# Kernel optimization log

Measured on AMD Instinct MI355X. Metric: run time of the kernel, lower is better.

Reference implementation:

```python
import jax, jax.numpy as jnp
import numpy as np

NUM_HEADS = 16


def setup_inputs() -> dict:
    key = jax.random.key(0)
    ks = jax.random.split(key, 9)
    B, N, C, R, T = 16, 1024, 1024, 64, 10
    s = 0.02
    x = jax.random.normal(ks[0], (B, N, C), dtype=jnp.float32)
    W_qkv = jax.random.normal(ks[1], (3 * C, C), dtype=jnp.float32) * s
    W_proj = jax.random.normal(ks[2], (C, C), dtype=jnp.float32) * s
    b_proj = jax.random.normal(ks[3], (C,), dtype=jnp.float32) * s
    A_k = jax.random.normal(ks[4], (T, R, C), dtype=jnp.float32) * s
    B_k = jax.random.normal(ks[5], (T, C, R), dtype=jnp.float32) * s
    A_v = jax.random.normal(ks[6], (T, R, C), dtype=jnp.float32) * s
    B_v = jax.random.normal(ks[7], (T, C, R), dtype=jnp.float32) * s
    return {"x": x, "W_qkv": W_qkv, "W_proj": W_proj, "b_proj": b_proj,
            "A_k": A_k, "B_k": B_k, "A_v": A_v, "B_v": B_v, "task": 4}


def reference(x, W_qkv, W_proj, b_proj, A_k, B_k, A_v, B_v, task):
    B, N, C = x.shape
    H = NUM_HEADS
    hd = C // H
    scale = hd ** (-0.5)

    # qkv projection: x @ W_qkv.T -> [B,N,3C] -> [3,B,H,N,hd]
    qkv = (x @ W_qkv.T).reshape(B, N, 3, H, hd).transpose(2, 0, 3, 1, 4)
    q, k, v = qkv[0], qkv[1], qkv[2]

    # merged LoRA weights: sum_{t<=task} B[t] @ A[t] -> [C, C]
    w_k = jnp.einsum('tcr,trd->cd', B_k[:task + 1], A_k[:task + 1])
    w_v = jnp.einsum('tcr,trd->cd', B_v[:task + 1], A_v[:task + 1])
    # F.linear(x, W) = x @ W.T ; reshape to [B,H,N,hd]
    dk = (x @ w_k.T).reshape(B, N, H, hd).transpose(0, 2, 1, 3)
    dv = (x @ w_v.T).reshape(B, N, H, hd).transpose(0, 2, 1, 3)
    k = k + dk
    v = v + dv

    attn = jax.nn.softmax(jnp.einsum('bhnd,bhmd->bhnm', q, k) * scale, axis=-1)
    out = jnp.einsum('bhnm,bhmd->bhnd', attn, v)
    out = out.transpose(0, 2, 1, 3).reshape(B, N, C)
    return out @ W_proj.T + b_proj
```

## Files before the change

### kernel.cpp

```cpp
#include <hip/hip_runtime.h>

typedef __attribute__((ext_vector_type(4))) float f32x4;
typedef __attribute__((ext_vector_type(8))) short s16x8;
typedef __attribute__((ext_vector_type(2))) unsigned int u32x2;
typedef __attribute__((ext_vector_type(4))) unsigned int u32x4;

#define LOG2E 1.44269504088896340736f

__device__ inline unsigned short f2b(float f) {
  unsigned int u = __float_as_uint(f);
  unsigned int r = (u + 0x7FFFu + ((u >> 16) & 1u)) >> 16;
  return (unsigned short)r;
}

__device__ inline unsigned int cvtpk_bf16(float lo, float hi) {
  unsigned int r;
  asm("v_cvt_pk_bf16_f32 %0, %1, %2" : "=v"(r) : "v"(lo), "v"(hi));
  return r;
}

__device__ inline void gload_lds16(const unsigned short* g, unsigned short* l) {
  __builtin_amdgcn_global_load_lds(
      (const __attribute__((address_space(1))) unsigned int*)g,
      (__attribute__((address_space(3))) unsigned int*)l, 16, 0, 0);
}

__global__ __launch_bounds__(256) void lora_merge(const float* __restrict__ A_k,
                                                  const float* __restrict__ B_k,
                                                  const float* __restrict__ A_v,
                                                  const float* __restrict__ B_v,
                                                  float* __restrict__ wk,
                                                  float* __restrict__ wv,
                                                  const int* __restrict__ taskp) {
  const float* A_ = blockIdx.y ? A_v : A_k;
  const float* B_ = blockIdx.y ? B_v : B_k;
  float* Wd = blockIdx.y ? wv : wk;
  __shared__ float Bs[64][65];
  __shared__ float As[64][65];
  const int tile = blockIdx.x;
  const int c0 = (tile >> 4) * 64, d0 = (tile & 15) * 64;
  const int tid = threadIdx.x;
  const int tx = tid & 15, ty = tid >> 4;
  const int T = *taskp + 1;
  float acc[4][4] = {};
  const int r = tid >> 2, cb = (tid & 3) * 16;
  for (int t = 0; t < T; ++t) {
    __syncthreads();
    const float* srcB = B_ + (size_t)t * 65536 + (size_t)(c0 + r) * 64 + cb;
    const float* srcA = A_ + (size_t)t * 65536 + (size_t)r * 1024 + d0 + cb;
#pragma unroll
    for (int j = 0; j < 16; j += 4) {
      f32x4 vb = *(const f32x4*)(srcB + j);
      Bs[r][cb + j] = vb.x; Bs[r][cb + j + 1] = vb.y;
      Bs[r][cb + j + 2] = vb.z; Bs[r][cb + j + 3] = vb.w;
      f32x4 va = *(const f32x4*)(srcA + j);
      As[r][cb + j] = va.x; As[r][cb + j + 1] = va.y;
      As[r][cb + j + 2] = va.z; As[r][cb + j + 3] = va.w;
    }
    __syncthreads();
#pragma unroll 8
    for (int rr = 0; rr < 64; ++rr) {
      float bv[4], av[4];
#pragma unroll
      for (int i = 0; i < 4; ++i) bv[i] = Bs[ty * 4 + i][rr];
#pragma unroll
      for (int j = 0; j < 4; ++j) av[j] = As[rr][tx * 4 + j];
#pragma unroll
      for (int i = 0; i < 4; ++i)
#pragma unroll
        for (int j = 0; j < 4; ++j) acc[i][j] += bv[i] * av[j];
    }
  }
#pragma unroll
  for (int i = 0; i < 4; ++i)
#pragma unroll
    for (int j = 0; j < 4; ++j)
      Wd[(size_t)(c0 + ty * 4 + i) * 1024 + d0 + tx * 4 + j] = acc[i][j];
}

__global__ void prep_all(const float* __restrict__ x, const float* __restrict__ Wproj,
                         const float* __restrict__ Wqkv, const float* __restrict__ wk,
                         const float* __restrict__ wv, unsigned short* __restrict__ xb,
                         unsigned short* __restrict__ Wp, unsigned short* __restrict__ Wc) {
  int i = blockIdx.x * 256 + threadIdx.x;
  f32x4 v;
  unsigned short* dst;
  int idx;
  if (i < 4194304) {
    idx = i; dst = xb;
    v = ((const f32x4*)x)[idx];
  } else if (i < 4456448) {
    idx = i - 4194304; dst = Wp;
    v = ((const f32x4*)Wproj)[idx];
  } else {
    idx = i - 4456448;
    dst = Wc;
    int e = idx * 4;
    v = *(const f32x4*)(Wqkv + e);
    int row = e >> 10;
    if (row >= 2048) {
      f32x4 d = *(const f32x4*)(wv + (e - 2097152));
      v = v + d;
    } else if (row >= 1024) {
      f32x4 d = *(const f32x4*)(wk + (e - 1048576));
      v = v + d;
    }
  }
  unsigned short o0 = f2b(v.x), o1 = f2b(v.y), o2 = f2b(v.z), o3 = f2b(v.w);
  unsigned long long pack = (unsigned long long)o0 | ((unsigned long long)o1 << 16) |
                            ((unsigned long long)o2 << 32) | ((unsigned long long)o3 << 48);
  ((unsigned long long*)dst)[idx] = pack;
}

template <int OUT_BF16, int ADD_BIAS, int VFUSE>
__global__ __launch_bounds__(512, 1) void gemm256(const unsigned short* __restrict__ A,
                                                  const unsigned short* __restrict__ B,
                                                  void* __restrict__ Cout,
                                                  const float* __restrict__ bias,
                                                  unsigned short* __restrict__ Vt,
                                                  int M, int N, int K) {
  __shared__ unsigned short SM[35840];
  const int tid = threadIdx.x;
  const int w = tid >> 6, l = tid & 63;
  const int lr = l & 15, lg = l >> 4;
  const int wm = w >> 2, wn = w & 3;

  const int lin = blockIdx.y * gridDim.x + blockIdx.x;
  const int cpx = (gridDim.x * gridDim.y) >> 3;
  const int s = (lin & 7) * cpx + (lin >> 3);
  const int bx = s % gridDim.x, by = s / gridDim.x;

  const int cs = tid ^ (((tid >> 5) & 1) << 1);
  const int r_st = ((cs >> 6) << 4) | ((cs >> 2) & 15);
  const int k_st = (cs & 3) << 3;
  const unsigned short* gA0 = A + (size_t)(by * 256 + r_st) * K + k_st;
  const unsigned short* gA1 = A + (size_t)(by * 256 + 128 + r_st) * K + k_st;
  const unsigned short* gB0 = B + (size_t)(bx * 256 + r_st) * K + k_st;
  const unsigned short* gB1 = B + (size_t)(bx * 256 + 128 + r_st) * K + k_st;
  const int wb = w * 512;

  const int swz = ((lr >> 3) & 1) << 4;
  const int fbase = lr * 32 + lg * 8;
  const int hA = wm * 4096;
  const int hB = (wn >> 1) * 4096;
  const int nb = (wn & 1) * 4;

  f32x4 acc[8][4] = {};
  const int NT = K >> 5;

#define SA_(t) (&SM[(t) * 8192])
#define SB_(t) (&SM[16384 + (t) * 8192])

  gload_lds16(gA0, SA_(0) + wb);
  gload_lds16(gA1, SA_(0) + 4096 + wb);
  gload_lds16(gB0, SB_(0) + wb);
  gload_lds16(gB1, SB_(0) + 4096 + wb);
  asm volatile("s_waitcnt vmcnt(0)" ::: "memory");
  __builtin_amdgcn_s_barrier();
  __builtin_amdgcn_sched_barrier(0);

  for (int t = 0; t < NT; ++t) {
    const int slot = t & 1;
    const int ts = (t + 1 < NT) ? (t + 1) : (NT - 1);
    const int ssl = (t + 1) & 1;
    const unsigned short* sa = SA_(slot) + hA;
    const unsigned short* sb = SB_(slot) + hB;
    gload_lds16(gA0 + ts * 32, SA_(ssl) + wb);
    gload_lds16(gA1 + ts * 32, SA_(ssl) + 4096 + wb);
    gload_lds16(gB0 + ts * 32, SB_(ssl) + wb);
    gload_lds16(gB1 + ts * 32, SB_(ssl) + 4096 + wb);
    s16x8 af[8], bf[2];
#pragma unroll
    for (int m = 0; m < 8; ++m)
      af[m] = *(const s16x8*)&sa[(m * 512 + fbase) ^ swz];
#pragma unroll
    for (int n = 0; n < 2; ++n)
      bf[n] = *(const s16x8*)&sb[((nb + n) * 512 + fbase) ^ swz];
    asm volatile("s_waitcnt lgkmcnt(0)" ::: "memory");
    __builtin_amdgcn_sched_barrier(0);
    __builtin_amdgcn_s_setprio(1);
#pragma unroll
    for (int m = 0; m < 8; ++m)
#pragma unroll
      for (int n = 0; n < 2; ++n)
        acc[m][n] = __builtin_amdgcn_mfma_f32_16x16x32_bf16(af[m], bf[n], acc[m][n], 0, 0, 0);
    __builtin_amdgcn_s_setprio(0);
    __builtin_amdgcn_sched_barrier(0);
#pragma unroll
    for (int n = 0; n < 2; ++n)
      bf[n] = *(const s16x8*)&sb[((nb + 2 + n) * 512 + fbase) ^ swz];
    asm volatile("s_waitcnt lgkmcnt(0)" ::: "memory");
    __builtin_amdgcn_sched_barrier(0);
    __builtin_amdgcn_s_setprio(1);
#pragma unroll
    for (int m = 0; m < 8; ++m)
#pragma unroll
      for (int n = 0; n < 2; ++n)
        acc[m][2 + n] = __builtin_amdgcn_mfma_f32_16x16x32_bf16(af[m], bf[n], acc[m][2 + n], 0, 0, 0);
    __builtin_amdgcn_s_setprio(0);
    __builtin_amdgcn_sched_barrier(0);
    asm volatile("s_waitcnt vmcnt(0)" ::: "memory");
    __builtin_amdgcn_s_barrier();
    __builtin_amdgcn_sched_barrier(0);
  }

  const int crow0 = by * 256 + wm * 128;
  const int ccol0 = bx * 256 + wn * 64;

  if (VFUSE) {
    unsigned short* Cq = (unsigned short*)Cout;
    if (bx < 8) {
      unsigned short* Cb = Cq + ((size_t)((ccol0 >> 10) & 1)) * 16777216;
#pragma unroll
      for (int m = 0; m < 8; ++m)
#pragma unroll
        for (int n = 0; n < 4; ++n)
#pragma unroll
          for (int rr = 0; rr < 4; ++rr) {
            int row = crow0 + m * 16 + lg * 4 + rr;
            int col = (ccol0 + n * 16 + lr) & 1023;
            Cb[(size_t)row * 1024 + col] = f2b(acc[m][n][rr]);
          }
    } else {
      asm volatile("s_waitcnt vmcnt(0)" ::: "memory");
      __syncthreads();
      unsigned int* T32 = (unsigned int*)SM;
      const int h0 = (bx - 8) * 4;
      const int bb = by >> 2;
      const int n_base = (by & 3) * 256;
#pragma unroll
      for (int hf = 0; hf < 2; ++hf) {
        if (wm == hf) {
#pragma unroll
          for (int m = 0; m < 8; ++m)
#pragma unroll
            for (int n = 0; n < 4; ++n) {
              int lcol = wn * 64 + n * 16 + lr;
              u32x2 pk;
              pk.x = (unsigned int)f2b(acc[m][n][0]) | ((unsigned int)f2b(acc[m][n][1]) << 16);
              pk.y = (unsigned int)f2b(acc[m][n][2]) | ((unsigned int)f2b(acc[m][n][3]) << 16);
              *(u32x2*)&T32[lcol * 68 + m * 8 + lg * 2] = pk;
            }
        }
        __syncthreads();
#pragma unroll
        for (int p = 0; p < 8; ++p) {
          int slot2 = p * 512 + tid;
          int d256 = slot2 >> 4;
          int ncq = (slot2 & 15) * 4;
          u32x4 v = *(const u32x4*)&T32[d256 * 68 + ncq];
          int hloc = d256 >> 6, d = d256 & 63;
          size_t dst = (size_t)(bb * 16 + h0 + hloc) * 65536 + (size_t)d * 1024 +
                       (n_base + hf * 128 + ncq * 2);
          *(u32x4*)&Vt[dst] = v;
        }
        __syncthreads();
      }
    }
  } else if (OUT_BF16) {
    unsigned short* C = (unsigned short*)Cout;
#pragma unroll
    for (int m = 0; m < 8; ++m)
#pragma unroll
      for (int n = 0; n < 4; ++n)
#pragma unroll
        for (int rr = 0; rr < 4; ++rr) {
          int row = crow0 + m * 16 + lg * 4 + rr;
          int col = ccol0 + n * 16 + lr;
          C[(size_t)row * N + col] = f2b(acc[m][n][rr]);
        }
  } else {
    float* C = (float*)Cout;
#pragma unroll
    for (int m = 0; m < 8; ++m)
#pragma unroll
      for (int n = 0; n < 4; ++n)
#pragma unroll
        for (int rr = 0; rr < 4; ++rr) {
          int row = crow0 + m * 16 + lg * 4 + rr;
          int col = ccol0 + n * 16 + lr;
          float b = ADD_BIAS ? bias[col] : 0.f;
          C[(size_t)row * N + col] = acc[m][n][rr] + b;
        }
  }
#undef SA_
#undef SB_
}

__global__ __launch_bounds__(512) void attn_fwd(const unsigned short* __restrict__ Qb,
                                                const unsigned short* __restrict__ Kb,
                                                const unsigned short* __restrict__ vT,
                                                unsigned short* __restrict__ out) {
  const int tid = threadIdx.x;
  const int w = tid >> 6, l = tid & 63;
  const int lr = l & 15, lg = l >> 4;
  const int bid = blockIdx.x;
  const int g = (bid & 7) * 32 + (bid >> 5);
  const int qt2 = (bid >> 3) & 3;
  const int b = g >> 4, h = g & 15;

  __shared__ unsigned short Ks[2][4096];
  __shared__ unsigned short Vs[2][4096];
  __shared__ unsigned int Ps[16][576];

  const size_t base = (size_t)b * 1048576 + h * 64;
  const unsigned short* Qp = Qb + base;
  const unsigned short* Kp = Kb + base;
  const unsigned short* vTp = vT + (size_t)(b * 16 + h) * 65536;

  const float SSCALE = 0.125f * LOG2E;
  const int qb = qt2 * 256;
  s16x8 qf[2][2];
#pragma unroll
  for (int qg = 0; qg < 2; ++qg) {
    const int qrow = qb + qg * 128 + w * 16 + lr;
    qf[qg][0] = *(const s16x8*)(Qp + (size_t)qrow * 1024 + lg * 8);
    qf[qg][1] = *(const s16x8*)(Qp + (size_t)qrow * 1024 + 32 + lg * 8);
#pragma unroll
    for (int kk = 0; kk < 2; ++kk)
#pragma unroll
      for (int j = 0; j < 8; ++j) {
        float f = __uint_as_float(((unsigned int)(unsigned short)qf[qg][kk][j]) << 16) * SSCALE;
        qf[qg][kk][j] = (short)f2b(f);
      }
  }

  s16x8 ONES;
#pragma unroll
  for (int j = 0; j < 8; ++j) ONES[j] = (short)0x3F80;

  f32x4 o[2][4] = {};
  f32x4 o4[2] = {};

  const int srow = tid >> 3;
  const int csrc = (tid & 7) ^ (srow & 7);

  gload_lds16(Kp + (size_t)srow * 1024 + csrc * 8, &Ks[0][w * 512]);
  gload_lds16(vTp + (size_t)srow * 1024 + csrc * 8, &Vs[0][w * 512]);
  __syncthreads();

  for (int t = 0; t < 16; ++t) {
    const int cur = t & 1;
    if (t < 15) {
      const int kv1 = (t + 1) * 64;
      gload_lds16(Kp + (size_t)(kv1 + srow) * 1024 + csrc * 8, &Ks[cur ^ 1][w * 512]);
      gload_lds16(vTp + (size_t)srow * 1024 + kv1 + csrc * 8, &Vs[cur ^ 1][w * 512]);
    }
    const unsigned short* Kb_ = &Ks[cur][0];
    const unsigned short* Vb = &Vs[cur][0];

    f32x4 sc[2][4] = {};
    __builtin_amdgcn_s_setprio(1);
#pragma unroll
    for (int kk = 0; kk < 2; ++kk)
#pragma unroll
      for (int tt = 0; tt < 4; ++tt) {
        int krow = tt * 16 + lr;
        s16x8 kf = *(const s16x8*)&Kb_[krow * 64 + ((((kk * 32 + lg * 8) >> 3) ^ (krow & 7)) << 3)];
        sc[0][tt] = __builtin_amdgcn_mfma_f32_16x16x32_bf16(kf, qf[0][kk], sc[0][tt], 0, 0, 0);
        sc[1][tt] = __builtin_amdgcn_mfma_f32_16x16x32_bf16(kf, qf[1][kk], sc[1][tt], 0, 0, 0);
      }
    __builtin_amdgcn_s_setprio(0);

#pragma unroll
    for (int qg = 0; qg < 2; ++qg) {
      unsigned int* Pw = &Ps[(w << 1) | qg][0];
#pragma unroll
      for (int tt = 0; tt < 4; ++tt) {
        float p0 = exp2f(sc[qg][tt][0]);
        float p1 = exp2f(sc[qg][tt][1]);
        float p2 = exp2f(sc[qg][tt][2]);
        float p3 = exp2f(sc[qg][tt][3]);
        u32x2 pk;
        pk.x = cvtpk_bf16(p0, p1);
        pk.y = cvtpk_bf16(p2, p3);
        *(u32x2*)&Pw[lr * 36 + tt * 8 + lg * 2] = pk;
      }
    }
    __builtin_amdgcn_sched_barrier(0);

#pragma unroll
    for (int kk = 0; kk < 2; ++kk) {
      u32x4 pu0 = *(const u32x4*)&Ps[(w << 1)][lr * 36 + kk * 16 + lg * 4];
      u32x4 pu1 = *(const u32x4*)&Ps[(w << 1) | 1][lr * 36 + kk * 16 + lg * 4];
      s16x8 pf0 = __builtin_bit_cast(s16x8, pu0);
      s16x8 pf1 = __builtin_bit_cast(s16x8, pu1);
      __builtin_amdgcn_s_setprio(1);
      o4[0] = __builtin_amdgcn_mfma_f32_16x16x32_bf16(pf0, ONES, o4[0], 0, 0, 0);
      o4[1] = __builtin_amdgcn_mfma_f32_16x16x32_bf16(pf1, ONES, o4[1], 0, 0, 0);
#pragma unroll
      for (int dt = 0; dt < 4; ++dt) {
        int vrow = dt * 16 + lr;
        s16x8 vf = *(const s16x8*)&Vb[vrow * 64 + ((((kk * 32 + lg * 8) >> 3) ^ (vrow & 7)) << 3)];
        o[0][dt] = __builtin_amdgcn_mfma_f32_16x16x32_bf16(pf0, vf, o[0][dt], 0, 0, 0);
        o[1][dt] = __builtin_amdgcn_mfma_f32_16x16x32_bf16(pf1, vf, o[1][dt], 0, 0, 0);
      }
      __builtin_amdgcn_s_setprio(0);
    }
    __syncthreads();
  }

#pragma unroll
  for (int qg = 0; qg < 2; ++qg) {
    f32x4 lq;
#pragma unroll
    for (int rr = 0; rr < 4; ++rr) lq[rr] = 1.f / o4[qg][rr];
    const size_t orow0 = (size_t)b * 1024 + qb + qg * 128 + w * 16;
#pragma unroll
    for (int dt = 0; dt < 4; ++dt)
#pragma unroll
      for (int rr = 0; rr < 4; ++rr)
        out[(orow0 + lg * 4 + rr) * 1024 + h * 64 + dt * 16 + lr] = f2b(o[qg][dt][rr] * lq[rr]);
  }
}

extern "C" void kernel_launch(void* const* d_in, const int* in_sizes, int n_in,
                              void* d_out, int out_size, void* d_ws, size_t ws_size,
                              hipStream_t stream) {
  const float* x = (const float*)d_in[0];
  const float* Wqkv = (const float*)d_in[1];
  const float* Wproj = (const float*)d_in[2];
  const float* bproj = (const float*)d_in[3];
  const float* A_k = (const float*)d_in[4];
  const float* B_k = (const float*)d_in[5];
  const float* A_v = (const float*)d_in[6];
  const float* B_v = (const float*)d_in[7];
  const int* task = (const int*)d_in[8];

  char* ws = (char*)d_ws;
  float* wk = (float*)ws;
  float* wv = (float*)(ws + (4ull << 20));
  unsigned short* xb = (unsigned short*)(ws + (8ull << 20));
  unsigned short* Wc = (unsigned short*)(ws + (40ull << 20));
  unsigned short* Wp = (unsigned short*)(ws + (46ull << 20));
  unsigned short* Qb = (unsigned short*)(ws + (48ull << 20));
  unsigned short* Kb = (unsigned short*)(ws + (80ull << 20));
  unsigned short* vT = (unsigned short*)(ws + (112ull << 20));
  unsigned short* ao = (unsigned short*)(ws + (144ull << 20));

  lora_merge<<<dim3(256, 2), 256, 0, stream>>>(A_k, B_k, A_v, B_v, wk, wv, task);
  prep_all<<<20480, 256, 0, stream>>>(x, Wproj, Wqkv, wk, wv, xb, Wp, Wc);
  gemm256<1, 0, 1><<<dim3(12, 64), 512, 0, stream>>>(xb, Wc, Qb, nullptr, vT, 16384, 3072, 1024);
  attn_fwd<<<1024, 512, 0, stream>>>(Qb, Kb, vT, ao);
  gemm256<0, 1, 0><<<dim3(4, 64), 512, 0, stream>>>(ao, Wp, d_out, bproj, nullptr, 16384, 1024, 1024);
}
```

Measured before the change: 315.4 us.

## Restructure GEMM main loop into 8-phase pipeline with deeper LDS buffering

The bf16 GEMM main loop moves from a 2-stage, 32-wide K double buffer to two 64-wide K buffers (128 KB LDS) processed in eight phases per iteration. Each phase interleaves one global→LDS load with an MFMA block, separated by barriers, and waits only partially on vmcnt. The aim is to keep more loads in flight and hide memory latency behind MFMA work instead of draining all loads every step. In exchange it adds many more barriers per iteration, and the larger LDS footprint rules out co-resident blocks.

```diff
diff --git a/kernel.cpp b/kernel.cpp
--- a/kernel.cpp
+++ b/kernel.cpp
@@ -24,6 +24,8 @@
       (const __attribute__((address_space(1))) unsigned int*)g,
       (__attribute__((address_space(3))) unsigned int*)l, 16, 0, 0);
 }
+
+#define MFMA16(a, b, c) __builtin_amdgcn_mfma_f32_16x16x32_bf16((a), (b), (c), 0, 0, 0)
 
 __global__ __launch_bounds__(256) void lora_merge(const float* __restrict__ A_k,
                                                   const float* __restrict__ B_k,
@@ -119,7 +121,7 @@
                                                   const float* __restrict__ bias,
                                                   unsigned short* __restrict__ Vt,
                                                   int M, int N, int K) {
-  __shared__ unsigned short SM[35840];
+  __shared__ unsigned short SM[65536];
   const int tid = threadIdx.x;
   const int w = tid >> 6, l = tid & 63;
   const int lr = l & 15, lg = l >> 4;
@@ -139,69 +141,127 @@
   const unsigned short* gB1 = B + (size_t)(bx * 256 + 128 + r_st) * K + k_st;
   const int wb = w * 512;
 
-  const int swz = ((lr >> 3) & 1) << 4;
-  const int fbase = lr * 32 + lg * 8;
-  const int hA = wm * 4096;
-  const int hB = (wn >> 1) * 4096;
+  const int fs = (lr * 32 + lg * 8) ^ (((lr >> 3) & 1) << 4);
+  const int A0 = wm * 8192;
+  const int B0 = 32768 + (wn >> 1) * 8192;
   const int nb = (wn & 1) * 4;
 
   f32x4 acc[8][4] = {};
-  const int NT = K >> 5;
-
-#define SA_(t) (&SM[(t) * 8192])
-#define SB_(t) (&SM[16384 + (t) * 8192])
-
-  gload_lds16(gA0, SA_(0) + wb);
-  gload_lds16(gA1, SA_(0) + 4096 + wb);
-  gload_lds16(gB0, SB_(0) + wb);
-  gload_lds16(gB1, SB_(0) + 4096 + wb);
-  asm volatile("s_waitcnt vmcnt(0)" ::: "memory");
+  const int NT2 = K >> 7;
+
+#define STA(bb, kt, kk)                                                          \
+  gload_lds16(gA0 + (kt) * 64 + (kk) * 32, &SM[(bb) * 16384 + (kk) * 4096 + wb]); \
+  gload_lds16(gA1 + (kt) * 64 + (kk) * 32, &SM[(bb) * 16384 + 8192 + (kk) * 4096 + wb]);
+#define STB(bb, kt, kk)                                                                   \
+  gload_lds16(gB0 + (kt) * 64 + (kk) * 32, &SM[32768 + (bb) * 16384 + (kk) * 4096 + wb]); \
+  gload_lds16(gB1 + (kt) * 64 + (kk) * 32, &SM[32768 + (bb) * 16384 + 8192 + (kk) * 4096 + wb]);
+#define PH_GATE                                            \
+  __builtin_amdgcn_s_barrier();                            \
+  asm volatile("s_waitcnt lgkmcnt(0)" ::: "memory");       \
+  __builtin_amdgcn_sched_barrier(0);                       \
+  __builtin_amdgcn_s_setprio(1);
+#define PH_END                                             \
+  __builtin_amdgcn_s_setprio(0);                           \
+  __builtin_amdgcn_sched_barrier(0);                       \
+  __builtin_amdgcn_s_barrier();
+#define PH_END_VM                                          \
+  __builtin_amdgcn_s_setprio(0);                           \
+  __builtin_amdgcn_sched_barrier(0);                       \
+  asm volatile("s_waitcnt vmcnt(6)" ::: "memory");         \
+  __builtin_amdgcn_s_barrier();                            \
+  __builtin_amdgcn_sched_barrier(0);
+
+  STA(0, 0, 0); STB(0, 0, 0); STA(0, 0, 1); STB(0, 0, 1);
+  STA(1, 1, 0); STB(1, 1, 0); STA(1, 1, 1);
+  asm volatile("s_waitcnt vmcnt(6)" ::: "memory");
   __builtin_amdgcn_s_barrier();
   __builtin_amdgcn_sched_barrier(0);
 
-  for (int t = 0; t < NT; ++t) {
-    const int slot = t & 1;
-    const int ts = (t + 1 < NT) ? (t + 1) : (NT - 1);
-    const int ssl = (t + 1) & 1;
-    const unsigned short* sa = SA_(slot) + hA;
-    const unsigned short* sb = SB_(slot) + hB;
-    gload_lds16(gA0 + ts * 32, SA_(ssl) + wb);
-    gload_lds16(gA1 + ts * 32, SA_(ssl) + 4096 + wb);
-    gload_lds16(gB0 + ts * 32, SB_(ssl) + wb);
-    gload_lds16(gB1 + ts * 32, SB_(ssl) + 4096 + wb);
+  for (int it = 0; it < NT2; ++it) {
+    const int kt1 = 2 * it + 1;
+    const int st2 = (it < NT2 - 1) ? 2 * it + 2 : 2 * it;
+    const int st3 = (it < NT2 - 1) ? 2 * it + 3 : 2 * it + 1;
     s16x8 af[8], bf[2];
 #pragma unroll
-    for (int m = 0; m < 8; ++m)
-      af[m] = *(const s16x8*)&sa[(m * 512 + fbase) ^ swz];
-#pragma unroll
-    for (int n = 0; n < 2; ++n)
-      bf[n] = *(const s16x8*)&sb[((nb + n) * 512 + fbase) ^ swz];
-    asm volatile("s_waitcnt lgkmcnt(0)" ::: "memory");
-    __builtin_amdgcn_sched_barrier(0);
-    __builtin_amdgcn_s_setprio(1);
-#pragma unroll
-    for (int m = 0; m < 8; ++m)
-#pragma unroll
-      for (int n = 0; n < 2; ++n)
-        acc[m][n] = __builtin_amdgcn_mfma_f32_16x16x32_bf16(af[m], bf[n], acc[m][n], 0, 0, 0);
-    __builtin_amdgcn_s_setprio(0);
-    __builtin_amdgcn_sched_barrier(0);
-#pragma unroll
-    for (int n = 0; n < 2; ++n)
-      bf[n] = *(const s16x8*)&sb[((nb + 2 + n) * 512 + fbase) ^ swz];
-    asm volatile("s_waitcnt lgkmcnt(0)" ::: "memory");
-    __builtin_amdgcn_sched_barrier(0);
-    __builtin_amdgcn_s_setprio(1);
-#pragma unroll
-    for (int m = 0; m < 8; ++m)
-#pragma unroll
-      for (int n = 0; n < 2; ++n)
-        acc[m][2 + n] = __builtin_amdgcn_mfma_f32_16x16x32_bf16(af[m], bf[n], acc[m][2 + n], 0, 0, 0);
-    __builtin_amdgcn_s_setprio(0);
-    __builtin_amdgcn_sched_barrier(0);
-    asm volatile("s_waitcnt vmcnt(0)" ::: "memory");
-    __builtin_amdgcn_s_barrier();
-    __builtin_amdgcn_sched_barrier(0);
+    for (int m = 0; m < 8; ++m) af[m] = *(const s16x8*)&SM[A0 + m * 512 + fs];
+#pragma unroll
+    for (int j = 0; j < 2; ++j) bf[j] = *(const s16x8*)&SM[B0 + (nb + j) * 512 + fs];
+    STB(1, kt1, 1);
+    PH_GATE
+#pragma unroll
+    for (int m = 0; m < 8; ++m)
+#pragma unroll
+      for (int j = 0; j < 2; ++j) acc[m][j] = MFMA16(af[m], bf[j], acc[m][j]);
+    PH_END
+#pragma unroll
+    for (int j = 0; j < 2; ++j) bf[j] = *(const s16x8*)&SM[B0 + (nb + 2 + j) * 512 + fs];
+    STA(0, st2, 0);
+    PH_GATE
+#pragma unroll
+    for (int m = 0; m < 8; ++m)
+#pragma unroll
+      for (int j = 0; j < 2; ++j) acc[m][2 + j] = MFMA16(af[m], bf[j], acc[m][2 + j]);
+    PH_END
+#pragma unroll
+    for (int m = 0; m < 8; ++m) af[m] = *(const s16x8*)&SM[A0 + 4096 + m * 512 + fs];
+#pragma unroll
+    for (int j = 0; j < 2; ++j) bf[j] = *(const s16x8*)&SM[B0 + 4096 + (nb + j) * 512 + fs];
+    STB(0, st2, 0);
+    PH_GATE
+#pragma unroll
+    for (int m = 0; m < 8; ++m)
+#pragma unroll
+      for (int j = 0; j < 2; ++j) acc[m][j] = MFMA16(af[m], bf[j], acc[m][j]);
+    PH_END
+#pragma unroll
+    for (int j = 0; j < 2; ++j) bf[j] = *(const s16x8*)&SM[B0 + 4096 + (nb + 2 + j) * 512 + fs];
+    STA(0, st2, 1);
+    PH_GATE
+#pragma unroll
+    for (int m = 0; m < 8; ++m)
+#pragma unroll
+      for (int j = 0; j < 2; ++j) acc[m][2 + j] = MFMA16(af[m], bf[j], acc[m][2 + j]);
+    PH_END_VM
+#pragma unroll
+    for (int m = 0; m < 8; ++m) af[m] = *(const s16x8*)&SM[16384 + A0 + m * 512 + fs];
+#pragma unroll
+    for (int j = 0; j < 2; ++j) bf[j] = *(const s16x8*)&SM[16384 + B0 + (nb + j) * 512 + fs];
+    STB(0, st2, 1);
+    PH_GATE
+#pragma unroll
+    for (int m = 0; m < 8; ++m)
+#pragma unroll
+      for (int j = 0; j < 2; ++j) acc[m][j] = MFMA16(af[m], bf[j], acc[m][j]);
+    PH_END
+#pragma unroll
+    for (int j = 0; j < 2; ++j) bf[j] = *(const s16x8*)&SM[16384 + B0 + (nb + 2 + j) * 512 + fs];
+    STA(1, st3, 0);
+    PH_GATE
+#pragma unroll
+    for (int m = 0; m < 8; ++m)
+#pragma unroll
+      for (int j = 0; j < 2; ++j) acc[m][2 + j] = MFMA16(af[m], bf[j], acc[m][2 + j]);
+    PH_END
+#pragma unroll
+    for (int m = 0; m < 8; ++m) af[m] = *(const s16x8*)&SM[16384 + A0 + 4096 + m * 512 + fs];
+#pragma unroll
+    for (int j = 0; j < 2; ++j) bf[j] = *(const s16x8*)&SM[16384 + B0 + 4096 + (nb + j) * 512 + fs];
+    STB(1, st3, 0);
+    PH_GATE
+#pragma unroll
+    for (int m = 0; m < 8; ++m)
+#pragma unroll
+      for (int j = 0; j < 2; ++j) acc[m][j] = MFMA16(af[m], bf[j], acc[m][j]);
+    PH_END
+#pragma unroll
+    for (int j = 0; j < 2; ++j) bf[j] = *(const s16x8*)&SM[16384 + B0 + 4096 + (nb + 2 + j) * 512 + fs];
+    STA(1, st3, 1);
+    PH_GATE
+#pragma unroll
+    for (int m = 0; m < 8; ++m)
+#pragma unroll
+      for (int j = 0; j < 2; ++j) acc[m][2 + j] = MFMA16(af[m], bf[j], acc[m][2 + j]);
+    PH_END_VM
   }
 
   const int crow0 = by * 256 + wm * 128;
@@ -283,8 +343,11 @@
           C[(size_t)row * N + col] = acc[m][n][rr] + b;
         }
   }
-#undef SA_
-#undef SB_
+#undef STA
+#undef STB
+#undef PH_GATE
+#undef PH_END
+#undef PH_END_VM
 }
 
 __global__ __launch_bounds__(512) void attn_fwd(const unsigned short* __restrict__ Qb,
@@ -357,8 +420,8 @@
       for (int tt = 0; tt < 4; ++tt) {
         int krow = tt * 16 + lr;
         s16x8 kf = *(const s16x8*)&Kb_[krow * 64 + ((((kk * 32 + lg * 8) >> 3) ^ (krow & 7)) << 3)];
-        sc[0][tt] = __builtin_amdgcn_mfma_f32_16x16x32_bf16(kf, qf[0][kk], sc[0][tt], 0, 0, 0);
-        sc[1][tt] = __builtin_amdgcn_mfma_f32_16x16x32_bf16(kf, qf[1][kk], sc[1][tt], 0, 0, 0);
+        sc[0][tt] = MFMA16(kf, qf[0][kk], sc[0][tt]);
+        sc[1][tt] = MFMA16(kf, qf[1][kk], sc[1][tt]);
       }
     __builtin_amdgcn_s_setprio(0);
 
@@ -386,14 +449,14 @@
       s16x8 pf0 = __builtin_bit_cast(s16x8, pu0);
       s16x8 pf1 = __builtin_bit_cast(s16x8, pu1);
       __builtin_amdgcn_s_setprio(1);
-      o4[0] = __builtin_amdgcn_mfma_f32_16x16x32_bf16(pf0, ONES, o4[0], 0, 0, 0);
-      o4[1] = __builtin_amdgcn_mfma_f32_16x16x32_bf16(pf1, ONES, o4[1], 0, 0, 0);
+      o4[0] = MFMA16(pf0, ONES, o4[0]);
+      o4[1] = MFMA16(pf1, ONES, o4[1]);
 #pragma unroll
       for (int dt = 0; dt < 4; ++dt) {
         int vrow = dt * 16 + lr;
         s16x8 vf = *(const s16x8*)&Vb[vrow * 64 + ((((kk * 32 + lg * 8) >> 3) ^ (vrow & 7)) << 3)];
-        o[0][dt] = __builtin_amdgcn_mfma_f32_16x16x32_bf16(pf0, vf, o[0][dt], 0, 0, 0);
-        o[1][dt] = __builtin_amdgcn_mfma_f32_16x16x32_bf16(pf1, vf, o[1][dt], 0, 0, 0);
+        o[0][dt] = MFMA16(pf0, vf, o[0][dt]);
+        o[1][dt] = MFMA16(pf1, vf, o[1][dt]);
       }
       __builtin_amdgcn_s_setprio(0);
     }
```

After: 312.0 us. No clear change (-1.1%).
